# Kernel tuning notes

Measured on AMD Instinct MI355X. Metric: run time of the kernel, lower is better.

## Reference

```python
import jax, jax.numpy as jnp
import numpy as np

N = 50000
E = 800000
P = 16
H = 128
NUM_LAYERS = 2


def _lin_params(key, fan_in, fan_out):
    k1, k2 = jax.random.split(key)
    bound = 1.0 / np.sqrt(fan_in)
    W = jax.random.uniform(k1, (fan_in, fan_out), jnp.float32, -bound, bound)
    b = jax.random.uniform(k2, (fan_out,), jnp.float32, -bound, bound)
    return W, b


def setup_inputs() -> dict:
    key = jax.random.key(0)
    ks = jax.random.split(key, 16)
    h = jax.random.normal(ks[0], (N, P), jnp.float32)
    x = jax.random.normal(ks[1], (N, 2), jnp.float32)
    edge_index = jax.random.randint(ks[2], (2, E), 0, N, jnp.int32)
    emb_W, emb_b = _lin_params(ks[3], P, H)
    e_W1, e_b1 = _lin_params(ks[4], 2 * H + 1, H)
    e_W2, e_b2 = _lin_params(ks[5], H, H)
    n_W1, n_b1 = _lin_params(ks[6], 2 * H, H)
    n_W2, n_b2 = _lin_params(ks[7], H, H)
    v_W1, v_b1 = _lin_params(ks[8], H, H)
    v_W2, v_b2 = _lin_params(ks[9], H, 2)
    c_W1, c_b1 = _lin_params(ks[10], H, H)
    c_W2, c_b2 = _lin_params(ks[11], H, 1)
    return dict(h=h, x=x, edge_index=edge_index,
                emb_W=emb_W, emb_b=emb_b,
                e_W1=e_W1, e_b1=e_b1, e_W2=e_W2, e_b2=e_b2,
                n_W1=n_W1, n_b1=n_b1, n_W2=n_W2, n_b2=n_b2,
                v_W1=v_W1, v_b1=v_b1, v_W2=v_W2, v_b2=v_b2,
                c_W1=c_W1, c_b1=c_b1, c_W2=c_W2, c_b2=c_b2)


def _mlp(z, W1, b1, W2, b2):
    return jnp.maximum(z @ W1 + b1, 0.0) @ W2 + b2


def reference(h, x, edge_index, emb_W, emb_b,
              e_W1, e_b1, e_W2, e_b2,
              n_W1, n_b1, n_W2, n_b2,
              v_W1, v_b1, v_W2, v_b2,
              c_W1, c_b1, c_W2, c_b2):
    row, col = edge_index[0], edge_index[1]
    n_nodes = h.shape[0]
    # edge count per source node for scatter-mean (0-count nodes stay 0)
    cnt = jax.ops.segment_sum(jnp.ones((row.shape[0],), h.dtype), row,
                              num_segments=n_nodes)
    denom = jnp.maximum(cnt, 1.0)[:, None]

    h = h @ emb_W + emb_b  # [N, H]
    v = None
    for _ in range(NUM_LAYERS):
        rel_pos = x[row] - x[col]                         # [E, 2]
        rel_dist = jnp.sum(rel_pos ** 2, axis=-1, keepdims=True)  # [E, 1]
        rel_theta = jnp.arctan2(rel_pos[:, 1], rel_pos[:, 0])     # [E]
        rel_pos2 = rel_dist * jnp.stack(
            [jnp.cos(2.0 * rel_theta), jnp.sin(2.0 * rel_theta)], axis=1)  # [E, 2]
        edge_feat = jnp.concatenate([h[row], h[col], rel_dist], axis=-1)   # [E, 2H+1]
        m_ij = _mlp(edge_feat, e_W1, e_b1, e_W2, e_b2)    # [E, H] (dropout = eval identity)
        m_i = jax.ops.segment_sum(m_ij, row, num_segments=n_nodes)  # [N, H]
        h = h + _mlp(jnp.concatenate([h, m_i], axis=-1), n_W1, n_b1, n_W2, n_b2)
        v = _mlp(h, v_W1, v_b1, v_W2, v_b2)               # [N, 2]
        coord = _mlp(m_ij, c_W1, c_b1, c_W2, c_b2)        # [E, 1]
        scat = jax.ops.segment_sum(rel_pos2 * coord, row, num_segments=n_nodes)
        v = v + scat / denom                              # scatter-mean
    # F.normalize(p=2, dim=-1, eps=1e-12)
    norm = jnp.linalg.norm(v, axis=-1, keepdims=True)
    v = v / jnp.maximum(norm, 1e-12)
    return h, x, v
```

## Files before the change

kernel.cpp:

```cpp
#include <hip/hip_runtime.h>

typedef _Float16 f16;
typedef unsigned short u16;
typedef f16 f16x8 __attribute__((ext_vector_type(8)));
typedef float f32x4 __attribute__((ext_vector_type(4)));

constexpr int N_NODES = 50000;
constexpr int E_EDGES = 800000;
constexpr int NBINS   = 50176;
constexpr int NBLK    = 196;

constexpr size_t OFF_DEG   = 0;
constexpr size_t OFF_LOCEX = 200704;
constexpr size_t OFF_BSUM  = 401408;
constexpr size_t OFF_BOFF  = 402432;
constexpr size_t OFF_FILL  = 403456;
constexpr size_t OFF_SCAT  = 604160;
constexpr size_t OFF_SROW  = 1004160;
constexpr size_t OFF_SCOL  = 2604160;
constexpr size_t OFF_ZSUM  = 4204160;
constexpr size_t ZS_BYTES  = (size_t)N_NODES * 128 * 4;
constexpr size_t OFF_APRE  = OFF_ZSUM + ZS_BYTES;
constexpr size_t OFF_BPRE  = OFF_APRE + (size_t)N_NODES * 128 * 2;
constexpr size_t OFF_CMB   = OFF_BPRE + (size_t)N_NODES * 128 * 2;
constexpr size_t OFF_WX    = OFF_CMB + 65536;
constexpr size_t OFF_BVEC  = OFF_WX + 65536;
constexpr size_t OFF_BX    = OFF_BVEC + 512;
constexpr size_t OFF_WSWZ  = OFF_BX + 512;

__device__ __forceinline__ void split_f(float x, f16& h, f16& l) {
    h = (f16)x;
    l = (f16)(x - (float)h);
}

__device__ __forceinline__ f32x4 mfma3(f16x8 ah, f16x8 al, f16x8 bh, f16x8 bl, f32x4 acc) {
    acc = __builtin_amdgcn_mfma_f32_16x16x32_f16(ah, bh, acc, 0, 0, 0);
    acc = __builtin_amdgcn_mfma_f32_16x16x32_f16(al, bh, acc, 0, 0, 0);
    acc = __builtin_amdgcn_mfma_f32_16x16x32_f16(ah, bl, acc, 0, 0, 0);
    return acc;
}

__global__ __launch_bounds__(256) void compose_kernel(
    const float* __restrict__ eW2, const float* __restrict__ eb2,
    const float* __restrict__ nW1, const float* __restrict__ cW1,
    const float* __restrict__ cb1,
    float* __restrict__ Wcmb, float* __restrict__ Wx,
    float* __restrict__ bvec, float* __restrict__ bx)
{
    const int gid = blockIdx.x * 256 + threadIdx.x;
    if (gid < 16384) {
        const int k = gid >> 7, j = gid & 127;
        float s = 0.f;
        for (int t2 = 0; t2 < 128; ++t2) s += eW2[k * 128 + t2] * nW1[(128 + t2) * 128 + j];
        Wcmb[gid] = s;
    } else if (gid < 32768) {
        const int e = gid - 16384;
        const int k = e >> 7, j = e & 127;
        float s = 0.f;
        for (int t2 = 0; t2 < 128; ++t2) s += eW2[k * 128 + t2] * cW1[t2 * 128 + j];
        Wx[e] = s;
    } else if (gid < 32896) {
        const int j = gid - 32768;
        float s = 0.f;
        for (int k = 0; k < 128; ++k) s += eb2[k] * nW1[(128 + k) * 128 + j];
        bvec[j] = s;
    } else if (gid < 33024) {
        const int j = gid - 32896;
        float s = cb1[j];
        for (int k = 0; k < 128; ++k) s += eb2[k] * cW1[k * 128 + j];
        bx[j] = s;
    }
}

__global__ __launch_bounds__(256) void prep_kernel(
    const float* __restrict__ eW1, const float* __restrict__ nW1,
    const float* __restrict__ nW2, const float* __restrict__ vW1,
    const float* __restrict__ Wcmb, const float* __restrict__ Wx,
    f16* __restrict__ Wpres, f16* __restrict__ nW1cs,
    f16* __restrict__ nW2s, f16* __restrict__ vW1s, f16* __restrict__ Wxs)
{
    const int gid = blockIdx.x * 256 + threadIdx.x;
    int K32, e, which; f16* out;
    if (gid < 32768)       { which = 0; out = Wpres; K32 = 4; e = gid; }
    else if (gid < 65536)  { which = 1; out = nW1cs; K32 = 8; e = gid - 32768; }
    else if (gid < 81920)  { which = 2; out = nW2s;  K32 = 4; e = gid - 65536; }
    else if (gid < 98304)  { which = 3; out = vW1s;  K32 = 4; e = gid - 81920; }
    else                   { which = 4; out = Wxs;   K32 = 4; e = gid - 98304; }
    const int per = 512 * K32;
    const int ct = e / per, rem = e % per;
    const int kk = rem >> 9, lane = (rem >> 3) & 63, j = rem & 7;
    const int col = ct * 16 + (lane & 15);
    const int k = kk * 32 + ((lane >> 4) & 3) * 8 + j;
    float v;
    if (which == 0)      v = (col < 128) ? eW1[k * 128 + col] : eW1[(128 + k) * 128 + (col - 128)];
    else if (which == 1) v = (k < 128) ? nW1[k * 128 + col] : Wcmb[(k - 128) * 128 + col];
    else if (which == 2) v = nW2[k * 128 + col];
    else if (which == 3) v = vW1[k * 128 + col];
    else                 v = Wx[k * 128 + col];
    f16 h, l; split_f(v, h, l);
    const int base = ((ct * K32 + kk) * 2) * 512 + lane * 8 + j;
    out[base] = h;
    out[base + 512] = l;
}

__global__ __launch_bounds__(256) void hist_kernel(const int* __restrict__ eidx,
                                                   int* __restrict__ deg) {
    const int e = blockIdx.x * 256 + threadIdx.x;
    if (e < E_EDGES) atomicAdd(&deg[eidx[e]], 1);
}

__global__ __launch_bounds__(256) void scan1_kernel(const int* __restrict__ deg,
                                                    int* __restrict__ locEx,
                                                    int* __restrict__ blockSum) {
    __shared__ int s[256];
    const int t = threadIdx.x;
    const int gid = blockIdx.x * 256 + t;
    const int v = deg[gid];
    s[t] = v;
    __syncthreads();
    for (int off = 1; off < 256; off <<= 1) {
        const int add = (t >= off) ? s[t - off] : 0;
        __syncthreads();
        s[t] += add;
        __syncthreads();
    }
    locEx[gid] = s[t] - v;
    if (t == 255) blockSum[blockIdx.x] = s[255];
}

__global__ __launch_bounds__(256) void scan2_kernel(const int* __restrict__ blockSum,
                                                    int* __restrict__ blockOff) {
    __shared__ int s[256];
    const int t = threadIdx.x;
    const int v = (t < NBLK) ? blockSum[t] : 0;
    s[t] = v;
    __syncthreads();
    for (int off = 1; off < 256; off <<= 1) {
        const int add = (t >= off) ? s[t - off] : 0;
        __syncthreads();
        s[t] += add;
        __syncthreads();
    }
    if (t < NBLK) blockOff[t] = s[t] - v;
}

__global__ __launch_bounds__(256) void scatter_kernel(const int* __restrict__ eidx,
        const int* __restrict__ locEx, const int* __restrict__ blockOff,
        int* __restrict__ fill, u16* __restrict__ srow, u16* __restrict__ scol) {
    const int e = blockIdx.x * 256 + threadIdx.x;
    if (e >= E_EDGES) return;
    const int r = eidx[e], c = eidx[E_EDGES + e];
    const int pos = blockOff[r >> 8] + locEx[r] + atomicAdd(&fill[r], 1);
    srow[pos] = (u16)r;
    scol[pos] = (u16)c;
}

__global__ __launch_bounds__(256) void embed_kernel(
    const float* __restrict__ h_in, const float* __restrict__ embW,
    const float* __restrict__ embb, float* __restrict__ h)
{
    const int gid = blockIdx.x * 256 + threadIdx.x;
    if (gid >= N_NODES * 128) return;
    const int n = gid >> 7, j = gid & 127;
    float s = embb[j];
#pragma unroll
    for (int p = 0; p < 16; ++p) s += h_in[n * 16 + p] * embW[p * 128 + j];
    h[gid] = s;
}

__device__ __forceinline__ void stage8(const float* src, f16* dst) {
    const float4 f0 = *(const float4*)src;
    const float4 f1 = *(const float4*)(src + 4);
    const float xs[8] = {f0.x, f0.y, f0.z, f0.w, f1.x, f1.y, f1.z, f1.w};
    f16x8 vh, vl;
#pragma unroll
    for (int i = 0; i < 8; ++i) { f16 hh, ll; split_f(xs[i], hh, ll); vh[i] = hh; vl[i] = ll; }
    *(f16x8*)dst = vh;
    *(f16x8*)(dst + 8) = vl;
}

__global__ __launch_bounds__(256, 4) void pre_kernel(
    const float* __restrict__ h, const f16* __restrict__ Wpres,
    const float* __restrict__ eb1,
    f16* __restrict__ Apre, f16* __restrict__ Bpre)
{
    constexpr int S = 264;
    __shared__ f16 smA[64 * S];
    const int t = threadIdx.x;
    const int base = blockIdx.x * 64;
    const int lane = t & 63, w = t >> 6, qq = lane >> 4, nn = lane & 15;

#pragma unroll
    for (int it = 0; it < 4; ++it) {
        const int idx = it * 256 + t;
        const int el = idx >> 4, seg = idx & 15;
        const int node = base + el;
        f16* dst = &smA[el * S + seg * 16];
        if (node < N_NODES) {
            stage8(h + (size_t)node * 128 + seg * 8, dst);
        } else {
            *(f16x8*)dst = (f16x8)(f16)0.f;
            *(f16x8*)(dst + 8) = (f16x8)(f16)0.f;
        }
    }
    __syncthreads();

#pragma unroll
    for (int half = 0; half < 2; ++half) {
        f32x4 acc[4][2] = {};
        for (int kk = 0; kk < 4; ++kk) {
            f16x8 Ah[4], Al[4];
#pragma unroll
            for (int rt = 0; rt < 4; ++rt) {
                const f16* ap = &smA[(rt * 16 + nn) * S + (kk * 4 + qq) * 16];
                Ah[rt] = *(const f16x8*)ap;
                Al[rt] = *(const f16x8*)(ap + 8);
            }
#pragma unroll
            for (int c = 0; c < 2; ++c) {
                const int ct = w * 4 + half * 2 + c;
                const f16* bp = Wpres + (size_t)((ct * 4 + kk) * 2) * 512 + lane * 8;
                const f16x8 Bh = *(const f16x8*)bp;
                const f16x8 Bl = *(const f16x8*)(bp + 512);
#pragma unroll
                for (int rt = 0; rt < 4; ++rt)
                    acc[rt][c] = mfma3(Ah[rt], Al[rt], Bh, Bl, acc[rt][c]);
            }
        }
#pragma unroll
        for (int c = 0; c < 2; ++c) {
            const int col = w * 64 + half * 32 + c * 16 + nn;
#pragma unroll
            for (int rt = 0; rt < 4; ++rt) {
#pragma unroll
                for (int r = 0; r < 4; ++r) {
                    const int el = rt * 16 + qq * 4 + r;
                    const int node = base + el;
                    if (node < N_NODES) {
                        const float v = acc[rt][c][r];
                        if (col < 128) Apre[(size_t)node * 128 + col] = (f16)(v + eb1[col]);
                        else           Bpre[(size_t)node * 128 + (col - 128)] = (f16)v;
                    }
                }
            }
        }
    }
}

__global__ __launch_bounds__(256, 4) void edge_kernel(
    const u16* __restrict__ srow, const u16* __restrict__ scol,
    const float* __restrict__ x,
    const f16* __restrict__ Apre, const f16* __restrict__ Bpre,
    const float* __restrict__ wlast,
    const f16* __restrict__ Wxs, const float* __restrict__ bx,
    const float* __restrict__ cW2, const float* __restrict__ cb2,
    float* __restrict__ zsum, float* __restrict__ scat, const int do_coord)
{
    constexpr int S = 264;
    __shared__ f16 smA[64 * S];
    __shared__ int smRow[64], smCol[64];
    __shared__ float smRd[64], smP2x[64], smP2y[64];
    __shared__ float smPart[4][64];

    const int t = threadIdx.x;
    const int base = blockIdx.x * 64;
    const int lane = t & 63, w = t >> 6, qq = lane >> 4, nn = lane & 15;

    if (t < 64) {
        const int e = base + t;
        const int r = (int)srow[e], c = (int)scol[e];
        smRow[t] = r;
        smCol[t] = c;
        const float dx = x[2 * r] - x[2 * c];
        const float dy = x[2 * r + 1] - x[2 * c + 1];
        smRd[t] = dx * dx + dy * dy;
        smP2x[t] = dx * dx - dy * dy;
        smP2y[t] = 2.0f * dx * dy;
    }
    __syncthreads();

#pragma unroll
    for (int it = 0; it < 4; ++it) {
        const int idx = it * 256 + t;
        const int el = idx >> 4, seg = idx & 15;
        const int rn = smRow[el], cn = smCol[el];
        const f16x8 av = *(const f16x8*)(Apre + (size_t)rn * 128 + seg * 8);
        const f16x8 bv = *(const f16x8*)(Bpre + (size_t)cn * 128 + seg * 8);
        const float4 w0 = *(const float4*)(wlast + seg * 8);
        const float4 w1 = *(const float4*)(wlast + seg * 8 + 4);
        const float rd = smRd[el];
        const float wl[8] = {w0.x, w0.y, w0.z, w0.w, w1.x, w1.y, w1.z, w1.w};
        f16x8 vh, vl;
#pragma unroll
        for (int i = 0; i < 8; ++i) {
            const float z = fmaxf((float)av[i] + (float)bv[i] + rd * wl[i], 0.f);
            f16 hh, ll; split_f(z, hh, ll);
            vh[i] = hh; vl[i] = ll;
        }
        f16* dst = &smA[el * S + seg * 16];
        *(f16x8*)dst = vh;
        *(f16x8*)(dst + 8) = vl;
    }
    __syncthreads();

    {
        const int col = t & 127;
        const int r0 = (t >> 7) * 32;
        const f16* mpBase = smA + (col >> 3) * 16 + (col & 7);
        float acc = 0.f;
        int prev = smRow[r0];
        for (int el = r0; el < r0 + 32; ++el) {
            const int rw = smRow[el];
            if (rw != prev) {
                atomicAdd(&zsum[(size_t)prev * 128 + col], acc);
                acc = 0.f; prev = rw;
            }
            const f16* mp = mpBase + el * S;
            acc += (float)mp[0] + (float)mp[8];
        }
        atomicAdd(&zsum[(size_t)prev * 128 + col], acc);
    }

    if (do_coord) {
        f32x4 acc3[4][2] = {};
        for (int kk = 0; kk < 4; ++kk) {
            f16x8 Ah[4], Al[4];
#pragma unroll
            for (int rt = 0; rt < 4; ++rt) {
                const f16* ap = &smA[(rt * 16 + nn) * S + (kk * 4 + qq) * 16];
                Ah[rt] = *(const f16x8*)ap;
                Al[rt] = *(const f16x8*)(ap + 8);
            }
#pragma unroll
            for (int c = 0; c < 2; ++c) {
                const int ct = w * 2 + c;
                const f16* bp = Wxs + (size_t)((ct * 4 + kk) * 2) * 512 + lane * 8;
                const f16x8 Bh = *(const f16x8*)bp;
                const f16x8 Bl = *(const f16x8*)(bp + 512);
#pragma unroll
                for (int rt = 0; rt < 4; ++rt)
                    acc3[rt][c] = mfma3(Ah[rt], Al[rt], Bh, Bl, acc3[rt][c]);
            }
        }
        float p3[4][4];
#pragma unroll
        for (int rt = 0; rt < 4; ++rt)
#pragma unroll
            for (int r = 0; r < 4; ++r) p3[rt][r] = 0.f;
#pragma unroll
        for (int c = 0; c < 2; ++c) {
            const int col = w * 32 + c * 16 + nn;
            const float c1 = bx[col];
            const float w2 = cW2[col];
#pragma unroll
            for (int rt = 0; rt < 4; ++rt)
#pragma unroll
                for (int r = 0; r < 4; ++r)
                    p3[rt][r] += fmaxf(acc3[rt][c][r] + c1, 0.f) * w2;
        }
#pragma unroll
        for (int off = 1; off < 16; off <<= 1)
#pragma unroll
            for (int rt = 0; rt < 4; ++rt)
#pragma unroll
                for (int r = 0; r < 4; ++r) p3[rt][r] += __shfl_xor(p3[rt][r], off);
        if (nn == 0) {
#pragma unroll
            for (int rt = 0; rt < 4; ++rt)
#pragma unroll
                for (int r = 0; r < 4; ++r)
                    smPart[w][rt * 16 + qq * 4 + r] = p3[rt][r];
        }
        __syncthreads();
        if (t < 64) {
            const float co = smPart[0][t] + smPart[1][t] + smPart[2][t] + smPart[3][t] + cb2[0];
            const int rw = smRow[t];
            atomicAdd(&scat[2 * rw],     smP2x[t] * co);
            atomicAdd(&scat[2 * rw + 1], smP2y[t] * co);
        }
    }
}

__global__ __launch_bounds__(256, 4) void node_kernel(
    float* __restrict__ h, const float* __restrict__ zsum,
    const int* __restrict__ deg,
    const f16* __restrict__ nW1cs, const float* __restrict__ nb1,
    const float* __restrict__ bvec,
    const f16* __restrict__ nW2s, const float* __restrict__ nb2)
{
    constexpr int S = 264;
    __shared__ f16 smA[64 * S];
    __shared__ float smDeg[64];
    const int t = threadIdx.x;
    const int base = blockIdx.x * 64;
    const int lane = t & 63, w = t >> 6, qq = lane >> 4, nn = lane & 15;

    if (t < 64) smDeg[t] = (float)deg[base + t];

    f32x4 acc1[4][2] = {};
    for (int chunk = 0; chunk < 2; ++chunk) {
        if (chunk) __syncthreads();
        const float* src0 = chunk == 0 ? h : zsum;
#pragma unroll
        for (int it = 0; it < 4; ++it) {
            const int idx = it * 256 + t;
            const int el = idx >> 4, seg = idx & 15;
            const int node = base + el;
            f16* dst = &smA[el * S + seg * 16];
            if (node < N_NODES) {
                stage8(src0 + (size_t)node * 128 + seg * 8, dst);
            } else {
                *(f16x8*)dst = (f16x8)(f16)0.f;
                *(f16x8*)(dst + 8) = (f16x8)(f16)0.f;
            }
        }
        __syncthreads();
        for (int kk = 0; kk < 4; ++kk) {
            f16x8 Ah[4], Al[4];
#pragma unroll
            for (int rt = 0; rt < 4; ++rt) {
                const f16* ap = &smA[(rt * 16 + nn) * S + (kk * 4 + qq) * 16];
                Ah[rt] = *(const f16x8*)ap;
                Al[rt] = *(const f16x8*)(ap + 8);
            }
            const int kkg = chunk * 4 + kk;
#pragma unroll
            for (int c = 0; c < 2; ++c) {
                const int ct = w * 2 + c;
                const f16* bp = nW1cs + (size_t)((ct * 8 + kkg) * 2) * 512 + lane * 8;
                const f16x8 Bh = *(const f16x8*)bp;
                const f16x8 Bl = *(const f16x8*)(bp + 512);
#pragma unroll
                for (int rt = 0; rt < 4; ++rt)
                    acc1[rt][c] = mfma3(Ah[rt], Al[rt], Bh, Bl, acc1[rt][c]);
            }
        }
    }
    __syncthreads();
#pragma unroll
    for (int c = 0; c < 2; ++c) {
        const int col = w * 32 + c * 16 + nn;
        const float b1 = nb1[col];
        const float bv = bvec[col];
#pragma unroll
        for (int rt = 0; rt < 4; ++rt) {
#pragma unroll
            for (int r = 0; r < 4; ++r) {
                const int el = rt * 16 + qq * 4 + r;
                const float z = fmaxf(acc1[rt][c][r] + b1 + smDeg[el] * bv, 0.f);
                f16 zh, zl; split_f(z, zh, zl);
                f16* zp = &smA[el * S + (col >> 3) * 16 + (col & 7)];
                zp[0] = zh; zp[8] = zl;
            }
        }
    }
    __syncthreads();

    f32x4 acc2[4][2] = {};
    for (int kk = 0; kk < 4; ++kk) {
        f16x8 Ah[4], Al[4];
#pragma unroll
        for (int rt = 0; rt < 4; ++rt) {
            const f16* ap = &smA[(rt * 16 + nn) * S + (kk * 4 + qq) * 16];
            Ah[rt] = *(const f16x8*)ap;
            Al[rt] = *(const f16x8*)(ap + 8);
        }
#pragma unroll
        for (int c = 0; c < 2; ++c) {
            const int ct = w * 2 + c;
            const f16* bp = nW2s + (size_t)((ct * 4 + kk) * 2) * 512 + lane * 8;
            const f16x8 Bh = *(const f16x8*)bp;
            const f16x8 Bl = *(const f16x8*)(bp + 512);
#pragma unroll
            for (int rt = 0; rt < 4; ++rt)
                acc2[rt][c] = mfma3(Ah[rt], Al[rt], Bh, Bl, acc2[rt][c]);
        }
    }
#pragma unroll
    for (int c = 0; c < 2; ++c) {
        const int col = w * 32 + c * 16 + nn;
        const float b2 = nb2[col];
#pragma unroll
        for (int rt = 0; rt < 4; ++rt) {
#pragma unroll
            for (int r = 0; r < 4; ++r) {
                const int el = rt * 16 + qq * 4 + r;
                const int node = base + el;
                if (node < N_NODES) {
                    const size_t ix = (size_t)node * 128 + col;
                    h[ix] = h[ix] + acc2[rt][c][r] + b2;
                }
            }
        }
    }
}

__global__ __launch_bounds__(256, 4) void final_kernel(
    const float* __restrict__ h, const float* __restrict__ x,
    const f16* __restrict__ vW1s, const float* __restrict__ vb1,
    const float* __restrict__ vW2, const float* __restrict__ vb2,
    const float* __restrict__ scat, const int* __restrict__ deg,
    float* __restrict__ out)
{
    constexpr int S = 264;
    __shared__ f16 smA[64 * S];
    const int t = threadIdx.x;
    const int base = blockIdx.x * 64;
    const int lane = t & 63, w = t >> 6, qq = lane >> 4, nn = lane & 15;

#pragma unroll
    for (int it = 0; it < 4; ++it) {
        const int idx = it * 256 + t;
        const int el = idx >> 4, seg = idx & 15;
        const int node = base + el;
        f16* dst = &smA[el * S + seg * 16];
        if (node < N_NODES) {
            stage8(h + (size_t)node * 128 + seg * 8, dst);
        } else {
            *(f16x8*)dst = (f16x8)(f16)0.f;
            *(f16x8*)(dst + 8) = (f16x8)(f16)0.f;
        }
    }
    __syncthreads();

    f32x4 acc1[4][2] = {};
    for (int kk = 0; kk < 4; ++kk) {
        f16x8 Ah[4], Al[4];
#pragma unroll
        for (int rt = 0; rt < 4; ++rt) {
            const f16* ap = &smA[(rt * 16 + nn) * S + (kk * 4 + qq) * 16];
            Ah[rt] = *(const f16x8*)ap;
            Al[rt] = *(const f16x8*)(ap + 8);
        }
#pragma unroll
        for (int c = 0; c < 2; ++c) {
            const int ct = w * 2 + c;
            const f16* bp = vW1s + (size_t)((ct * 4 + kk) * 2) * 512 + lane * 8;
            const f16x8 Bh = *(const f16x8*)bp;
            const f16x8 Bl = *(const f16x8*)(bp + 512);
#pragma unroll
            for (int rt = 0; rt < 4; ++rt)
                acc1[rt][c] = mfma3(Ah[rt], Al[rt], Bh, Bl, acc1[rt][c]);
        }
    }
    __syncthreads();
#pragma unroll
    for (int c = 0; c < 2; ++c) {
        const int col = w * 32 + c * 16 + nn;
        const float b1 = vb1[col];
#pragma unroll
        for (int rt = 0; rt < 4; ++rt) {
#pragma unroll
            for (int r = 0; r < 4; ++r) {
                const int el = rt * 16 + qq * 4 + r;
                const float z = fmaxf(acc1[rt][c][r] + b1, 0.f);
                f16 zh, zl; split_f(z, zh, zl);
                f16* zp = &smA[el * S + (col >> 3) * 16 + (col & 7)];
                zp[0] = zh; zp[8] = zl;
            }
        }
    }
    __syncthreads();

    float* out_x = out + (size_t)N_NODES * 128;
    float* out_v = out_x + (size_t)N_NODES * 2;
    if (t < 128) {
        const int node = base + (t >> 1);
        if (node < N_NODES) out_x[node * 2 + (t & 1)] = x[node * 2 + (t & 1)];
    }
    if (t < 128) {
        const int rl = t >> 1, comp = t & 1;
        const int node = base + rl;
        float s = 0.f;
        if (node < N_NODES) {
            s = vb2[comp];
            for (int k = 0; k < 128; ++k) {
                const f16* zp = &smA[rl * S + (k >> 3) * 16 + (k & 7)];
                const float z = (float)zp[0] + (float)zp[8];
                s += z * vW2[k * 2 + comp];
            }
            const float dn = fmaxf((float)deg[node], 1.0f);
            s += scat[node * 2 + comp] / dn;
        }
        const float other = __shfl_xor(s, 1);
        if (node < N_NODES) {
            const float nrm = sqrtf(s * s + other * other);
            out_v[node * 2 + comp] = s / fmaxf(nrm, 1e-12f);
        }
    }
}

extern "C" void kernel_launch(void* const* d_in, const int* in_sizes, int n_in,
                              void* d_out, int out_size, void* d_ws, size_t ws_size,
                              hipStream_t stream) {
    const float* h_in = (const float*)d_in[0];
    const float* x    = (const float*)d_in[1];
    const int*   eidx = (const int*)d_in[2];
    const float* embW = (const float*)d_in[3];
    const float* embb = (const float*)d_in[4];
    const float* eW1  = (const float*)d_in[5];
    const float* eb1  = (const float*)d_in[6];
    const float* eW2  = (const float*)d_in[7];
    const float* eb2  = (const float*)d_in[8];
    const float* nW1  = (const float*)d_in[9];
    const float* nb1  = (const float*)d_in[10];
    const float* nW2  = (const float*)d_in[11];
    const float* nb2  = (const float*)d_in[12];
    const float* vW1  = (const float*)d_in[13];
    const float* vb1  = (const float*)d_in[14];
    const float* vW2  = (const float*)d_in[15];
    const float* vb2  = (const float*)d_in[16];
    const float* cW1  = (const float*)d_in[17];
    const float* cb1  = (const float*)d_in[18];
    const float* cW2  = (const float*)d_in[19];
    const float* cb2  = (const float*)d_in[20];

    char* ws = (char*)d_ws;
    int* deg    = (int*)(ws + OFF_DEG);
    int* locEx  = (int*)(ws + OFF_LOCEX);
    int* bsum   = (int*)(ws + OFF_BSUM);
    int* boff   = (int*)(ws + OFF_BOFF);
    int* fill   = (int*)(ws + OFF_FILL);
    float* scat = (float*)(ws + OFF_SCAT);
    u16* srow   = (u16*)(ws + OFF_SROW);
    u16* scol   = (u16*)(ws + OFF_SCOL);
    float* zsum = (float*)(ws + OFF_ZSUM);
    f16* Apre   = (f16*)(ws + OFF_APRE);
    f16* Bpre   = (f16*)(ws + OFF_BPRE);
    float* Wcmb = (float*)(ws + OFF_CMB);
    float* Wx   = (float*)(ws + OFF_WX);
    float* bvec = (float*)(ws + OFF_BVEC);
    float* bx   = (float*)(ws + OFF_BX);
    f16* Wpres  = (f16*)(ws + OFF_WSWZ);
    f16* nW1cs  = Wpres + 65536;
    f16* nW2s   = nW1cs + 65536;
    f16* vW1s   = nW2s + 32768;
    f16* Wxs    = vW1s + 32768;

    float* hcur = (float*)d_out;

    hipMemsetAsync(ws, 0, OFF_SROW, stream);
    hipMemsetAsync(zsum, 0, ZS_BYTES, stream);

    compose_kernel<<<129, 256, 0, stream>>>(eW2, eb2, nW1, cW1, cb1, Wcmb, Wx, bvec, bx);
    prep_kernel<<<448, 256, 0, stream>>>(eW1, nW1, nW2, vW1, Wcmb, Wx,
                                         Wpres, nW1cs, nW2s, vW1s, Wxs);
    hist_kernel<<<(E_EDGES + 255) / 256, 256, 0, stream>>>(eidx, deg);
    scan1_kernel<<<NBLK, 256, 0, stream>>>(deg, locEx, bsum);
    scan2_kernel<<<1, 256, 0, stream>>>(bsum, boff);
    scatter_kernel<<<(E_EDGES + 255) / 256, 256, 0, stream>>>(eidx, locEx, boff,
                                                              fill, srow, scol);
    embed_kernel<<<(N_NODES * 128 + 255) / 256, 256, 0, stream>>>(h_in, embW, embb, hcur);

    const float* wlast = eW1 + 256 * 128;

    pre_kernel<<<(N_NODES + 63) / 64, 256, 0, stream>>>(hcur, Wpres, eb1, Apre, Bpre);
    edge_kernel<<<E_EDGES / 64, 256, 0, stream>>>(srow, scol, x, Apre, Bpre, wlast,
        Wxs, bx, cW2, cb2, zsum, scat, 0);
    node_kernel<<<(N_NODES + 63) / 64, 256, 0, stream>>>(hcur, zsum, deg,
        nW1cs, nb1, bvec, nW2s, nb2);

    hipMemsetAsync(zsum, 0, ZS_BYTES, stream);

    pre_kernel<<<(N_NODES + 63) / 64, 256, 0, stream>>>(hcur, Wpres, eb1, Apre, Bpre);
    edge_kernel<<<E_EDGES / 64, 256, 0, stream>>>(srow, scol, x, Apre, Bpre, wlast,
        Wxs, bx, cW2, cb2, zsum, scat, 1);
    node_kernel<<<(N_NODES + 63) / 64, 256, 0, stream>>>(hcur, zsum, deg,
        nW1cs, nb1, bvec, nW2s, nb2);

    final_kernel<<<(N_NODES + 63) / 64, 256, 0, stream>>>(hcur, x,
        vW1s, vb1, vW2, vb2, scat, deg, (float*)d_out);
}
```

Before: 652.3 us.

## Split edge kernel, sum ReLU activations in registers, fold zsum clear into node kernel

Adds a lightweight edge_z_kernel for layer one that skips the shared-memory staging and instead accumulates the ReLU hidden activations in registers, with segmented atomics per run of equal source rows. The coord variant also accumulates zsum in registers during staging, which removes the second pass over shared memory. The node kernel now zeroes zsum after reading it, so the memset between layers is dropped. The trade-off is more atomics, since each thread covers only 4 edges, and extra write traffic in node_kernel.

```diff
diff --git a/kernel.cpp b/kernel.cpp
--- a/kernel.cpp
+++ b/kernel.cpp
@@ -247,14 +247,66 @@
     }
 }
 
-__global__ __launch_bounds__(256, 4) void edge_kernel(
+__global__ __launch_bounds__(256, 6) void edge_z_kernel(
+    const u16* __restrict__ srow, const u16* __restrict__ scol,
+    const float* __restrict__ x,
+    const f16* __restrict__ Apre, const f16* __restrict__ Bpre,
+    const float* __restrict__ wlast,
+    float* __restrict__ zsum)
+{
+    __shared__ int smRow[64], smCol[64];
+    __shared__ float smRd[64];
+    const int t = threadIdx.x;
+    const int base = blockIdx.x * 64;
+    if (t < 64) {
+        const int e = base + t;
+        const int r = (int)srow[e], c = (int)scol[e];
+        smRow[t] = r; smCol[t] = c;
+        const float dx = x[2 * r] - x[2 * c];
+        const float dy = x[2 * r + 1] - x[2 * c + 1];
+        smRd[t] = dx * dx + dy * dy;
+    }
+    __syncthreads();
+
+    const int g = t >> 4, seg = t & 15;
+    const float4 w0 = *(const float4*)(wlast + seg * 8);
+    const float4 w1 = *(const float4*)(wlast + seg * 8 + 4);
+    const float wl[8] = {w0.x, w0.y, w0.z, w0.w, w1.x, w1.y, w1.z, w1.w};
+
+    float acc[8] = {0.f, 0.f, 0.f, 0.f, 0.f, 0.f, 0.f, 0.f};
+    int prev = smRow[g * 4];
+#pragma unroll
+    for (int it = 0; it < 4; ++it) {
+        const int el = g * 4 + it;
+        const int rn = smRow[el], cn = smCol[el];
+        if (rn != prev) {
+#pragma unroll
+            for (int i = 0; i < 8; ++i)
+                atomicAdd(&zsum[(size_t)prev * 128 + seg * 8 + i], acc[i]);
+#pragma unroll
+            for (int i = 0; i < 8; ++i) acc[i] = 0.f;
+            prev = rn;
+        }
+        const f16x8 av = *(const f16x8*)(Apre + (size_t)rn * 128 + seg * 8);
+        const f16x8 bv = *(const f16x8*)(Bpre + (size_t)cn * 128 + seg * 8);
+        const float rd = smRd[el];
+#pragma unroll
+        for (int i = 0; i < 8; ++i)
+            acc[i] += fmaxf((float)av[i] + (float)bv[i] + rd * wl[i], 0.f);
+    }
+#pragma unroll
+    for (int i = 0; i < 8; ++i)
+        atomicAdd(&zsum[(size_t)prev * 128 + seg * 8 + i], acc[i]);
+}
+
+__global__ __launch_bounds__(256, 4) void edge_coord_kernel(
     const u16* __restrict__ srow, const u16* __restrict__ scol,
     const float* __restrict__ x,
     const f16* __restrict__ Apre, const f16* __restrict__ Bpre,
     const float* __restrict__ wlast,
     const f16* __restrict__ Wxs, const float* __restrict__ bx,
     const float* __restrict__ cW2, const float* __restrict__ cb2,
-    float* __restrict__ zsum, float* __restrict__ scat, const int do_coord)
+    float* __restrict__ zsum, float* __restrict__ scat)
 {
     constexpr int S = 264;
     __shared__ f16 smA[64 * S];
@@ -269,8 +321,7 @@
     if (t < 64) {
         const int e = base + t;
         const int r = (int)srow[e], c = (int)scol[e];
-        smRow[t] = r;
-        smCol[t] = c;
+        smRow[t] = r; smCol[t] = c;
         const float dx = x[2 * r] - x[2 * c];
         const float dy = x[2 * r + 1] - x[2 * c + 1];
         smRd[t] = dx * dx + dy * dy;
@@ -279,21 +330,33 @@
     }
     __syncthreads();
 
+    const int g = t >> 4, seg = t & 15;
+    const float4 w0 = *(const float4*)(wlast + seg * 8);
+    const float4 w1 = *(const float4*)(wlast + seg * 8 + 4);
+    const float wl[8] = {w0.x, w0.y, w0.z, w0.w, w1.x, w1.y, w1.z, w1.w};
+
+    float acc[8] = {0.f, 0.f, 0.f, 0.f, 0.f, 0.f, 0.f, 0.f};
+    int prev = smRow[g * 4];
 #pragma unroll
     for (int it = 0; it < 4; ++it) {
-        const int idx = it * 256 + t;
-        const int el = idx >> 4, seg = idx & 15;
+        const int el = g * 4 + it;
         const int rn = smRow[el], cn = smCol[el];
+        if (rn != prev) {
+#pragma unroll
+            for (int i = 0; i < 8; ++i)
+                atomicAdd(&zsum[(size_t)prev * 128 + seg * 8 + i], acc[i]);
+#pragma unroll
+            for (int i = 0; i < 8; ++i) acc[i] = 0.f;
+            prev = rn;
+        }
         const f16x8 av = *(const f16x8*)(Apre + (size_t)rn * 128 + seg * 8);
         const f16x8 bv = *(const f16x8*)(Bpre + (size_t)cn * 128 + seg * 8);
-        const float4 w0 = *(const float4*)(wlast + seg * 8);
-        const float4 w1 = *(const float4*)(wlast + seg * 8 + 4);
         const float rd = smRd[el];
-        const float wl[8] = {w0.x, w0.y, w0.z, w0.w, w1.x, w1.y, w1.z, w1.w};
         f16x8 vh, vl;
 #pragma unroll
         for (int i = 0; i < 8; ++i) {
             const float z = fmaxf((float)av[i] + (float)bv[i] + rd * wl[i], 0.f);
+            acc[i] += z;
             f16 hh, ll; split_f(z, hh, ll);
             vh[i] = hh; vl[i] = ll;
         }
@@ -301,88 +364,71 @@
         *(f16x8*)dst = vh;
         *(f16x8*)(dst + 8) = vl;
     }
-    __syncthreads();
-
-    {
-        const int col = t & 127;
-        const int r0 = (t >> 7) * 32;
-        const f16* mpBase = smA + (col >> 3) * 16 + (col & 7);
-        float acc = 0.f;
-        int prev = smRow[r0];
-        for (int el = r0; el < r0 + 32; ++el) {
-            const int rw = smRow[el];
-            if (rw != prev) {
-                atomicAdd(&zsum[(size_t)prev * 128 + col], acc);
-                acc = 0.f; prev = rw;
-            }
-            const f16* mp = mpBase + el * S;
-            acc += (float)mp[0] + (float)mp[8];
-        }
-        atomicAdd(&zsum[(size_t)prev * 128 + col], acc);
-    }
-
-    if (do_coord) {
-        f32x4 acc3[4][2] = {};
-        for (int kk = 0; kk < 4; ++kk) {
-            f16x8 Ah[4], Al[4];
-#pragma unroll
-            for (int rt = 0; rt < 4; ++rt) {
-                const f16* ap = &smA[(rt * 16 + nn) * S + (kk * 4 + qq) * 16];
-                Ah[rt] = *(const f16x8*)ap;
-                Al[rt] = *(const f16x8*)(ap + 8);
-            }
-#pragma unroll
-            for (int c = 0; c < 2; ++c) {
-                const int ct = w * 2 + c;
-                const f16* bp = Wxs + (size_t)((ct * 4 + kk) * 2) * 512 + lane * 8;
-                const f16x8 Bh = *(const f16x8*)bp;
-                const f16x8 Bl = *(const f16x8*)(bp + 512);
-#pragma unroll
-                for (int rt = 0; rt < 4; ++rt)
-                    acc3[rt][c] = mfma3(Ah[rt], Al[rt], Bh, Bl, acc3[rt][c]);
-            }
-        }
-        float p3[4][4];
+#pragma unroll
+    for (int i = 0; i < 8; ++i)
+        atomicAdd(&zsum[(size_t)prev * 128 + seg * 8 + i], acc[i]);
+    __syncthreads();
+
+    f32x4 acc3[4][2] = {};
+    for (int kk = 0; kk < 4; ++kk) {
+        f16x8 Ah[4], Al[4];
+#pragma unroll
+        for (int rt = 0; rt < 4; ++rt) {
+            const f16* ap = &smA[(rt * 16 + nn) * S + (kk * 4 + qq) * 16];
+            Ah[rt] = *(const f16x8*)ap;
+            Al[rt] = *(const f16x8*)(ap + 8);
+        }
+#pragma unroll
+        for (int c = 0; c < 2; ++c) {
+            const int ct = w * 2 + c;
+            const f16* bp = Wxs + (size_t)((ct * 4 + kk) * 2) * 512 + lane * 8;
+            const f16x8 Bh = *(const f16x8*)bp;
+            const f16x8 Bl = *(const f16x8*)(bp + 512);
+#pragma unroll
+            for (int rt = 0; rt < 4; ++rt)
+                acc3[rt][c] = mfma3(Ah[rt], Al[rt], Bh, Bl, acc3[rt][c]);
+        }
+    }
+    float p3[4][4];
+#pragma unroll
+    for (int rt = 0; rt < 4; ++rt)
+#pragma unroll
+        for (int r = 0; r < 4; ++r) p3[rt][r] = 0.f;
+#pragma unroll
+    for (int c = 0; c < 2; ++c) {
+        const int col = w * 32 + c * 16 + nn;
+        const float c1 = bx[col];
+        const float w2 = cW2[col];
 #pragma unroll
         for (int rt = 0; rt < 4; ++rt)
 #pragma unroll
-            for (int r = 0; r < 4; ++r) p3[rt][r] = 0.f;
-#pragma unroll
-        for (int c = 0; c < 2; ++c) {
-            const int col = w * 32 + c * 16 + nn;
-            const float c1 = bx[col];
-            const float w2 = cW2[col];
-#pragma unroll
-            for (int rt = 0; rt < 4; ++rt)
-#pragma unroll
-                for (int r = 0; r < 4; ++r)
-                    p3[rt][r] += fmaxf(acc3[rt][c][r] + c1, 0.f) * w2;
-        }
-#pragma unroll
-        for (int off = 1; off < 16; off <<= 1)
-#pragma unroll
-            for (int rt = 0; rt < 4; ++rt)
-#pragma unroll
-                for (int r = 0; r < 4; ++r) p3[rt][r] += __shfl_xor(p3[rt][r], off);
-        if (nn == 0) {
-#pragma unroll
-            for (int rt = 0; rt < 4; ++rt)
-#pragma unroll
-                for (int r = 0; r < 4; ++r)
-                    smPart[w][rt * 16 + qq * 4 + r] = p3[rt][r];
-        }
-        __syncthreads();
-        if (t < 64) {
-            const float co = smPart[0][t] + smPart[1][t] + smPart[2][t] + smPart[3][t] + cb2[0];
-            const int rw = smRow[t];
-            atomicAdd(&scat[2 * rw],     smP2x[t] * co);
-            atomicAdd(&scat[2 * rw + 1], smP2y[t] * co);
-        }
+            for (int r = 0; r < 4; ++r)
+                p3[rt][r] += fmaxf(acc3[rt][c][r] + c1, 0.f) * w2;
+    }
+#pragma unroll
+    for (int off = 1; off < 16; off <<= 1)
+#pragma unroll
+        for (int rt = 0; rt < 4; ++rt)
+#pragma unroll
+            for (int r = 0; r < 4; ++r) p3[rt][r] += __shfl_xor(p3[rt][r], off);
+    if (nn == 0) {
+#pragma unroll
+        for (int rt = 0; rt < 4; ++rt)
+#pragma unroll
+            for (int r = 0; r < 4; ++r)
+                smPart[w][rt * 16 + qq * 4 + r] = p3[rt][r];
+    }
+    __syncthreads();
+    if (t < 64) {
+        const float co = smPart[0][t] + smPart[1][t] + smPart[2][t] + smPart[3][t] + cb2[0];
+        const int rw = smRow[t];
+        atomicAdd(&scat[2 * rw],     smP2x[t] * co);
+        atomicAdd(&scat[2 * rw + 1], smP2y[t] * co);
     }
 }
 
 __global__ __launch_bounds__(256, 4) void node_kernel(
-    float* __restrict__ h, const float* __restrict__ zsum,
+    float* __restrict__ h, float* __restrict__ zsum,
     const int* __restrict__ deg,
     const f16* __restrict__ nW1cs, const float* __restrict__ nb1,
     const float* __restrict__ bvec,
@@ -400,7 +446,6 @@
     f32x4 acc1[4][2] = {};
     for (int chunk = 0; chunk < 2; ++chunk) {
         if (chunk) __syncthreads();
-        const float* src0 = chunk == 0 ? h : zsum;
 #pragma unroll
         for (int it = 0; it < 4; ++it) {
             const int idx = it * 256 + t;
@@ -408,7 +453,15 @@
             const int node = base + el;
             f16* dst = &smA[el * S + seg * 16];
             if (node < N_NODES) {
-                stage8(src0 + (size_t)node * 128 + seg * 8, dst);
+                if (chunk == 0) {
+                    stage8(h + (size_t)node * 128 + seg * 8, dst);
+                } else {
+                    float* src = zsum + (size_t)node * 128 + seg * 8;
+                    stage8(src, dst);
+                    const float4 zz = {0.f, 0.f, 0.f, 0.f};
+                    *(float4*)src = zz;
+                    *(float4*)(src + 4) = zz;
+                }
             } else {
                 *(f16x8*)dst = (f16x8)(f16)0.f;
                 *(f16x8*)(dst + 8) = (f16x8)(f16)0.f;
@@ -655,16 +708,13 @@
     const float* wlast = eW1 + 256 * 128;
 
     pre_kernel<<<(N_NODES + 63) / 64, 256, 0, stream>>>(hcur, Wpres, eb1, Apre, Bpre);
-    edge_kernel<<<E_EDGES / 64, 256, 0, stream>>>(srow, scol, x, Apre, Bpre, wlast,
-        Wxs, bx, cW2, cb2, zsum, scat, 0);
+    edge_z_kernel<<<E_EDGES / 64, 256, 0, stream>>>(srow, scol, x, Apre, Bpre, wlast, zsum);
     node_kernel<<<(N_NODES + 63) / 64, 256, 0, stream>>>(hcur, zsum, deg,
         nW1cs, nb1, bvec, nW2s, nb2);
 
-    hipMemsetAsync(zsum, 0, ZS_BYTES, stream);
-
     pre_kernel<<<(N_NODES + 63) / 64, 256, 0, stream>>>(hcur, Wpres, eb1, Apre, Bpre);
-    edge_kernel<<<E_EDGES / 64, 256, 0, stream>>>(srow, scol, x, Apre, Bpre, wlast,
-        Wxs, bx, cW2, cb2, zsum, scat, 1);
+    edge_coord_kernel<<<E_EDGES / 64, 256, 0, stream>>>(srow, scol, x, Apre, Bpre, wlast,
+        Wxs, bx, cW2, cb2, zsum, scat);
     node_kernel<<<(N_NODES + 63) / 64, 256, 0, stream>>>(hcur, zsum, deg,
         nW1cs, nb1, bvec, nW2s, nb2);
 
```

Measured after the change: 2.445 ms. +274.9%, slower.
